# Performance work log

Hardware: AMD Instinct MI355X
Metric: run time of the kernel (lower is better)

## Reference

```python
import jax, jax.numpy as jnp
import numpy as np

# CrossAttention (DFFNet): 1x1 convs produce q,k from depth and v from rgb;
# full dense attention over hw spatial tokens: softmax(q^T k) then v @ mask^T.

def setup_inputs() -> dict:
    key = jax.random.key(0)
    ks = jax.random.split(key, 8)
    B, C, H, W = 4, 256, 64, 64
    Cqk = C // 8  # ratio=8 -> 32
    s = 0.02
    return {
        "rgb":   jax.random.normal(ks[0], (B, C, H, W), jnp.float32),
        "depth": jax.random.normal(ks[1], (B, C, H, W), jnp.float32),
        "Wq": jax.random.normal(ks[2], (Cqk, C), jnp.float32) * s,
        "bq": jax.random.normal(ks[3], (Cqk,), jnp.float32) * s,
        "Wk": jax.random.normal(ks[4], (Cqk, C), jnp.float32) * s,
        "bk": jax.random.normal(ks[5], (Cqk,), jnp.float32) * s,
        "Wv": jax.random.normal(ks[6], (C, C), jnp.float32) * s,
        "bv": jax.random.normal(ks[7], (C,), jnp.float32) * s,
    }


def reference(rgb, depth, Wq, bq, Wk, bk, Wv, bv):
    B, C, H, W = rgb.shape
    hw = H * W
    d = depth.reshape(B, C, hw)   # [B, C, hw]
    r = rgb.reshape(B, C, hw)     # [B, C, hw]
    # 1x1 convs == channel-mixing linear maps
    q = jnp.einsum('oc,bcn->bon', Wq, d) + bq[None, :, None]  # [B, Cqk, hw]
    k = jnp.einsum('oc,bcn->bon', Wk, d) + bk[None, :, None]  # [B, Cqk, hw]
    v = jnp.einsum('oc,bcn->bon', Wv, r) + bv[None, :, None]  # [B, C, hw]
    # scores: q^T k -> [B, hw, hw], softmax over last dim
    scores = jnp.einsum('bcn,bcm->bnm', q, k)
    mask = jax.nn.softmax(scores, axis=-1)
    # feat = v @ mask^T  -> [B, C, hw]
    feat = jnp.einsum('bcm,bnm->bcn', v, mask)
    return feat.reshape(B, C, H, W)
```

## Files before the change

### kernel.cpp

```cpp
#include <hip/hip_runtime.h>
#include <stdint.h>

#define L2E 1.44269504088896340736f

typedef _Float16 half8 __attribute__((ext_vector_type(8)));
typedef float floatx4 __attribute__((ext_vector_type(4)));

static __device__ __forceinline__ unsigned short f32_to_f16u(float f) {
  union { _Float16 h; unsigned short s; } cv; cv.h = (_Float16)f; return cv.s;
}

static __device__ __forceinline__ float fast_exp2(float x) {
  float r;
  asm("v_exp_f32 %0, %1" : "=v"(r) : "v"(x));
  return r;
}

typedef __attribute__((address_space(3))) unsigned int as3_uint;
typedef __attribute__((address_space(1))) const unsigned int as1_cuint;

static __device__ __forceinline__ void async16(const void* g, void* l) {
  __builtin_amdgcn_global_load_lds((as1_cuint*)g, (as3_uint*)l, 16, 0, 0);
}

__global__ __launch_bounds__(256) void proj_kernel(
    const float* __restrict__ rgb,
    const float* __restrict__ depth,
    const float* __restrict__ Wq, const float* __restrict__ bq,
    const float* __restrict__ Wk, const float* __restrict__ bk,
    const float* __restrict__ Wv, const float* __restrict__ bv,
    unsigned short* __restrict__ qT,
    unsigned short* __restrict__ kT,
    unsigned short* __restrict__ v)
{
  __shared__ __align__(16) unsigned short sX[256 * 76];
  __shared__ __align__(16) unsigned short sW[32 * 256];

  const int n0 = blockIdx.x * 64;
  const int b  = blockIdx.y;
  const int z  = blockIdx.z;
  const int t  = threadIdx.x;
  const int w  = t >> 6;
  const int lane = t & 63;
  const int l15 = lane & 15;
  const int q4  = lane >> 4;

  const float* X = (z == 0) ? depth : rgb;
  const float* xb = X + (size_t)b * 256 * 4096 + n0;

#pragma unroll
  for (int i = 0; i < 8; i++) {
    int h = i * 256 + t;
    int c = h >> 3, oct = h & 7;
    const float* src = xb + (size_t)c * 4096 + oct * 8;
    float4 x0 = *(const float4*)src;
    float4 x1 = *(const float4*)(src + 4);
    half8 hh;
    hh[0] = (_Float16)x0.x; hh[1] = (_Float16)x0.y; hh[2] = (_Float16)x0.z; hh[3] = (_Float16)x0.w;
    hh[4] = (_Float16)x1.x; hh[5] = (_Float16)x1.y; hh[6] = (_Float16)x1.z; hh[7] = (_Float16)x1.w;
    *(half8*)&sX[c * 76 + oct * 8] = hh;
  }
  __syncthreads();

  half8 a8[8];
#pragma unroll
  for (int ks = 0; ks < 8; ks++) {
#pragma unroll
    for (int j = 0; j < 8; j++) {
      a8[ks][j] = *(const _Float16*)&sX[(ks * 32 + q4 * 8 + j) * 76 + 16 * w + l15];
    }
  }

  const int ns = (z == 0) ? 2 : 4;
  for (int s = 0; s < ns; s++) {
    const int colbase = (z == 0) ? 0 : (z - 1) * 128 + s * 32;
    __syncthreads();

#pragma unroll
    for (int i = 0; i < 4; i++) {
      int L = i * 256 + t;
      int og = L >> 5;
      int phys = L & 31;
      int ci = phys ^ (og & 7);
      const float* wr;
      if (z == 0) wr = ((s == 0) ? Wq : Wk) + (size_t)og * 256;
      else        wr = Wv + (size_t)(colbase + og) * 256;
      float4 w0 = *(const float4*)(wr + ci * 8);
      float4 w1 = *(const float4*)(wr + ci * 8 + 4);
      half8 h;
      h[0] = (_Float16)w0.x; h[1] = (_Float16)w0.y; h[2] = (_Float16)w0.z; h[3] = (_Float16)w0.w;
      h[4] = (_Float16)w1.x; h[5] = (_Float16)w1.y; h[6] = (_Float16)w1.z; h[7] = (_Float16)w1.w;
      *(half8*)&sW[(size_t)L * 8] = h;
    }

    float bias2[2];
#pragma unroll
    for (int ct = 0; ct < 2; ct++) {
      int og = ct * 16 + l15;
      if (z == 0) bias2[ct] = (s == 0) ? bq[og] : bk[og];
      else        bias2[ct] = bv[colbase + og];
    }
    __syncthreads();

    floatx4 acc2[2];
    acc2[0] = (floatx4){0.f, 0.f, 0.f, 0.f};
    acc2[1] = (floatx4){0.f, 0.f, 0.f, 0.f};

#pragma unroll
    for (int ks = 0; ks < 8; ks++) {
      const int ci = ks * 4 + q4;
#pragma unroll
      for (int ct = 0; ct < 2; ct++) {
        int og = ct * 16 + l15;
        half8 bf = *(const half8*)&sW[og * 256 + ((ci ^ (og & 7)) * 8)];
        acc2[ct] = __builtin_amdgcn_mfma_f32_16x16x32_f16(a8[ks], bf, acc2[ct], 0, 0, 0);
      }
    }

    __syncthreads();

    if (z == 0) {
#pragma unroll
      for (int ct = 0; ct < 2; ct++) {
        int og = ct * 16 + l15;
#pragma unroll
        for (int r = 0; r < 4; r++) {
          int n = n0 + 16 * w + q4 * 4 + r;
          unsigned short hv = f32_to_f16u(acc2[ct][r] + bias2[ct]);
          if (s == 0) qT[((size_t)b * 4096 + n) * 32 + og] = hv;
          else        kT[((size_t)b * 4096 + n) * 32 + og] = hv;
        }
      }
    } else {
      unsigned short* tile = sW;
#pragma unroll
      for (int ct = 0; ct < 2; ct++) {
#pragma unroll
        for (int r = 0; r < 4; r++) {
          int co_l = ct * 16 + l15;
          int nl = 16 * w + q4 * 4 + r;
          tile[co_l * 72 + nl] = f32_to_f16u(acc2[ct][r] + bias2[ct]);
        }
      }
      __syncthreads();
      {
        int co_l = t >> 3;
        int ch = t & 7;
        int4 val = *(const int4*)&tile[co_l * 72 + ch * 8];
        *(int4*)&v[((size_t)b * 256 + colbase + co_l) * 4096 + n0 + ch * 8] = val;
      }
    }
  }
}

static __device__ __forceinline__ void stage_v(
    const unsigned short* __restrict__ vB, unsigned char* sbase,
    int m0, int t, int w)
{
#pragma unroll
  for (int j = 0; j < 4; j++) {
    int lin = j * 256 + t;
    int c = lin >> 2;
    int p = lin & 3;
    int lc = p ^ ((c >> 1) & 3);
    async16(&vB[(size_t)c * 4096 + m0 + lc * 8], sbase + j * 4096 + w * 1024);
  }
}

__global__ __launch_bounds__(256, 4) void attn_kernel(
    const unsigned short* __restrict__ qT,
    const unsigned short* __restrict__ kT,
    const unsigned short* __restrict__ v,
    unsigned short* __restrict__ Op,
    float* __restrict__ lW)
{
  __shared__ __align__(16) unsigned char smem[37888];
  unsigned short* sP = (unsigned short*)(smem + 32768);

  const int o = blockIdx.x;
  const int n0 = ((o >> 3) & 63) * 64;
  const int p  = (o & 7) | ((o >> 9) << 3);
  const int b  = p & 3;
  const int chunk = p >> 2;
  const int t  = threadIdx.x;
  const int w  = t >> 6;
  const int lane = t & 63;
  const int l15 = lane & 15;
  const int q4  = lane >> 4;

  half8 aq = *(const half8*)(qT + ((size_t)b * 4096 + n0 + 16 * w + l15) * 32 + q4 * 8);

  const unsigned short* vB = v + (size_t)b * 256 * 4096;
  const unsigned short* kL = kT + (size_t)b * 4096 * 32 + (size_t)l15 * 32 + q4 * 8;
  unsigned short* sPw = sP + w * 640;

  float lsum[4] = {0.f, 0.f, 0.f, 0.f};
  floatx4 acc[16];
#pragma unroll
  for (int ct = 0; ct < 16; ct++) acc[ct] = (floatx4){0.f, 0.f, 0.f, 0.f};
  const floatx4 zf = (floatx4){0.f, 0.f, 0.f, 0.f};

  const int mbase = chunk * 1024;

  stage_v(vB, smem, mbase, t, w);
  half8 kc0 = *(const half8*)(kL + (size_t)mbase * 32);
  half8 kc1 = *(const half8*)(kL + (size_t)(mbase + 16) * 32);

  int bufoff = 0;
  for (int it = 0; it < 32; ++it) {
    const int m0 = mbase + it * 32;
    half8 kn0 = kc0, kn1 = kc1;
    if (it < 31) {
      stage_v(vB, smem + (bufoff ^ 16384), m0 + 32, t, w);
      kn0 = *(const half8*)(kL + (size_t)(m0 + 32) * 32);
      kn1 = *(const half8*)(kL + (size_t)(m0 + 48) * 32);
      asm volatile("s_waitcnt vmcnt(6)" ::: "memory");
    } else {
      asm volatile("s_waitcnt vmcnt(0)" ::: "memory");
    }

    floatx4 s0 = __builtin_amdgcn_mfma_f32_16x16x32_f16(aq, kc0, zf, 0, 0, 0);
    floatx4 s1 = __builtin_amdgcn_mfma_f32_16x16x32_f16(aq, kc1, zf, 0, 0, 0);

    float p0[4], p1[4];
#pragma unroll
    for (int r = 0; r < 4; r++) {
      p0[r] = fast_exp2(s0[r] * L2E);
      p1[r] = fast_exp2(s1[r] * L2E);
      lsum[r] += p0[r] + p1[r];
    }
#pragma unroll
    for (int r = 0; r < 4; r++) {
      int row = q4 * 4 + r;
      sPw[row * 40 + l15]      = f32_to_f16u(p0[r]);
      sPw[row * 40 + 16 + l15] = f32_to_f16u(p1[r]);
    }
    asm volatile("s_waitcnt lgkmcnt(0)" ::: "memory");

    __builtin_amdgcn_s_barrier();
    asm volatile("s_waitcnt lgkmcnt(0)" ::: "memory");

    half8 ap[4];
#pragma unroll
    for (int nt = 0; nt < 4; nt++)
      ap[nt] = *(const half8*)&sP[nt * 640 + l15 * 40 + q4 * 8];

    const unsigned short* sVb = (const unsigned short*)(smem + bufoff);
#pragma unroll
    for (int ct = 0; ct < 4; ct++) {
      int co = w * 64 + ct * 16 + l15;
      half8 bv8 = *(const half8*)&sVb[co * 32 + ((q4 ^ ((co >> 1) & 3)) * 8)];
#pragma unroll
      for (int nt = 0; nt < 4; nt++)
        acc[ct * 4 + nt] = __builtin_amdgcn_mfma_f32_16x16x32_f16(ap[nt], bv8, acc[ct * 4 + nt], 0, 0, 0);
    }
    asm volatile("s_waitcnt lgkmcnt(0)" ::: "memory");
    __builtin_amdgcn_s_barrier();

    kc0 = kn0; kc1 = kn1;
    bufoff ^= 16384;
  }

#pragma unroll
  for (int off = 1; off < 16; off <<= 1) {
#pragma unroll
    for (int r = 0; r < 4; r++) lsum[r] += __shfl_xor(lsum[r], off);
  }
  if (l15 == 0) {
#pragma unroll
    for (int r = 0; r < 4; r++)
      lW[((size_t)chunk * 4 + b) * 4096 + n0 + 16 * w + q4 * 4 + r] = lsum[r];
  }

  unsigned short* sO = (unsigned short*)smem;
#pragma unroll
  for (int pass = 0; pass < 2; pass++) {
    __syncthreads();
    if ((w >> 1) == pass) {
#pragma unroll
      for (int ct = 0; ct < 4; ct++) {
        int co_l = (w & 1) * 64 + ct * 16 + l15;
#pragma unroll
        for (int nt = 0; nt < 4; nt++) {
#pragma unroll
          for (int r = 0; r < 4; r++) {
            int nl = nt * 16 + q4 * 4 + r;
            sO[co_l * 72 + nl] = f32_to_f16u(acc[ct * 4 + nt][r]);
          }
        }
      }
    }
    __syncthreads();
#pragma unroll
    for (int s = 0; s < 4; s++) {
      int co_l = s * 32 + (t >> 3);
      int ch = t & 7;
      int4 val = *(const int4*)&sO[co_l * 72 + ch * 8];
      *(int4*)&Op[(((size_t)chunk * 4 + b) * 256 + pass * 128 + co_l) * 4096 + n0 + ch * 8] = val;
    }
  }
}

__global__ __launch_bounds__(256) void combine_kernel(
    const unsigned short* __restrict__ Op,
    const float* __restrict__ lW,
    float* __restrict__ out)
{
  const int t = threadIdx.x;
  const int b = blockIdx.y;
  const size_t n8 = (size_t)blockIdx.x * 2048 + (size_t)t * 8;
  const int co0 = blockIdx.z * 4;

  float sum[8] = {0.f, 0.f, 0.f, 0.f, 0.f, 0.f, 0.f, 0.f};
#pragma unroll
  for (int ch = 0; ch < 4; ch++) {
    const float* lp = lW + ((size_t)ch * 4 + b) * 4096 + n8;
    float4 a0 = *(const float4*)lp;
    float4 a1 = *(const float4*)(lp + 4);
    sum[0] += a0.x; sum[1] += a0.y; sum[2] += a0.z; sum[3] += a0.w;
    sum[4] += a1.x; sum[5] += a1.y; sum[6] += a1.z; sum[7] += a1.w;
  }
  float rl[8];
#pragma unroll
  for (int i = 0; i < 8; i++) rl[i] = 1.0f / sum[i];

#pragma unroll
  for (int cc = 0; cc < 4; cc++) {
    int co = co0 + cc;
    float o[8] = {0.f, 0.f, 0.f, 0.f, 0.f, 0.f, 0.f, 0.f};
#pragma unroll
    for (int ch = 0; ch < 4; ch++) {
      half8 hv = *(const half8*)&Op[(((size_t)ch * 4 + b) * 256 + co) * 4096 + n8];
#pragma unroll
      for (int i = 0; i < 8; i++) o[i] += (float)hv[i];
    }
    float* op = out + ((size_t)b * 256 + co) * 4096 + n8;
    float4 r0, r1;
    r0.x = o[0] * rl[0]; r0.y = o[1] * rl[1]; r0.z = o[2] * rl[2]; r0.w = o[3] * rl[3];
    r1.x = o[4] * rl[4]; r1.y = o[5] * rl[5]; r1.z = o[6] * rl[6]; r1.w = o[7] * rl[7];
    *(float4*)op = r0;
    *(float4*)(op + 4) = r1;
  }
}

extern "C" void kernel_launch(void* const* d_in, const int* in_sizes, int n_in,
                              void* d_out, int out_size, void* d_ws, size_t ws_size,
                              hipStream_t stream) {
  const float* rgb   = (const float*)d_in[0];
  const float* depth = (const float*)d_in[1];
  const float* Wq    = (const float*)d_in[2];
  const float* bq    = (const float*)d_in[3];
  const float* Wk    = (const float*)d_in[4];
  const float* bk    = (const float*)d_in[5];
  const float* Wv    = (const float*)d_in[6];
  const float* bv    = (const float*)d_in[7];
  float* out = (float*)d_out;

  unsigned short* qT = (unsigned short*)d_ws;
  unsigned short* kT = qT + (size_t)4 * 4096 * 32;
  unsigned short* vW = kT + (size_t)4 * 4096 * 32;
  unsigned short* Op = vW + (size_t)4 * 256 * 4096;
  float* lW = (float*)(Op + (size_t)4 * 4 * 256 * 4096);

  dim3 pg(64, 4, 3);
  proj_kernel<<<pg, 256, 0, stream>>>(rgb, depth, Wq, bq, Wk, bk, Wv, bv, qT, kT, vW);
  attn_kernel<<<dim3(1024, 1, 1), 256, 0, stream>>>(qT, kT, vW, Op, lW);
  dim3 cg(2, 4, 64);
  combine_kernel<<<cg, 256, 0, stream>>>(Op, lW, out);
}
```

Measured before the change: 160.3 us.

## Keep softmax probabilities in registers by transposing QK MFMA, drop P shared-memory roundtrip

Computes the score tile as K·Q so each lane's exp outputs already sit in the operand layout of a 16x16x16 MFMA. The probabilities then feed the PV product straight from registers instead of going through a shared-memory P buffer. Each wave now covers all 256 output channels for its own 16 query rows, with one barrier per iteration instead of two. The tradeoffs are twice as many smaller MFMAs, more V reads from shared memory per wave, and a full vmcnt(0) wait at the top of each iteration, which weakens the prefetch overlap.

```diff
diff --git a/kernel.cpp b/kernel.cpp
--- a/kernel.cpp
+++ b/kernel.cpp
@@ -4,6 +4,7 @@
 #define L2E 1.44269504088896340736f
 
 typedef _Float16 half8 __attribute__((ext_vector_type(8)));
+typedef _Float16 half4 __attribute__((ext_vector_type(4)));
 typedef float floatx4 __attribute__((ext_vector_type(4)));
 
 static __device__ __forceinline__ unsigned short f32_to_f16u(float f) {
@@ -174,8 +175,7 @@
     unsigned short* __restrict__ Op,
     float* __restrict__ lW)
 {
-  __shared__ __align__(16) unsigned char smem[37888];
-  unsigned short* sP = (unsigned short*)(smem + 32768);
+  __shared__ __align__(16) unsigned char smem[36864];
 
   const int o = blockIdx.x;
   const int n0 = ((o >> 3) & 63) * 64;
@@ -192,9 +192,8 @@
 
   const unsigned short* vB = v + (size_t)b * 256 * 4096;
   const unsigned short* kL = kT + (size_t)b * 4096 * 32 + (size_t)l15 * 32 + q4 * 8;
-  unsigned short* sPw = sP + w * 640;
-
-  float lsum[4] = {0.f, 0.f, 0.f, 0.f};
+
+  float lsum = 0.f;
   floatx4 acc[16];
 #pragma unroll
   for (int ct = 0; ct < 16; ct++) acc[ct] = (floatx4){0.f, 0.f, 0.f, 0.f};
@@ -206,98 +205,67 @@
   half8 kc0 = *(const half8*)(kL + (size_t)mbase * 32);
   half8 kc1 = *(const half8*)(kL + (size_t)(mbase + 16) * 32);
 
-  int bufoff = 0;
+  const int sw = (l15 >> 1) & 3;
+  const int offA = (((q4 >> 1) ^ sw) << 3) + ((q4 & 1) << 2);
+  const int offB = ((((q4 >> 1) + 2) ^ sw) << 3) + ((q4 & 1) << 2);
+
   for (int it = 0; it < 32; ++it) {
     const int m0 = mbase + it * 32;
-    half8 kn0 = kc0, kn1 = kc1;
+    asm volatile("s_waitcnt vmcnt(0)" ::: "memory");
+    __builtin_amdgcn_s_barrier();
+    asm volatile("" ::: "memory");
+
+    if (it < 31) stage_v(vB, smem + ((~it & 1) << 14), m0 + 32, t, w);
+
+    floatx4 s0 = __builtin_amdgcn_mfma_f32_16x16x32_f16(kc0, aq, zf, 0, 0, 0);
+    floatx4 s1 = __builtin_amdgcn_mfma_f32_16x16x32_f16(kc1, aq, zf, 0, 0, 0);
     if (it < 31) {
-      stage_v(vB, smem + (bufoff ^ 16384), m0 + 32, t, w);
-      kn0 = *(const half8*)(kL + (size_t)(m0 + 32) * 32);
-      kn1 = *(const half8*)(kL + (size_t)(m0 + 48) * 32);
-      asm volatile("s_waitcnt vmcnt(6)" ::: "memory");
-    } else {
-      asm volatile("s_waitcnt vmcnt(0)" ::: "memory");
-    }
-
-    floatx4 s0 = __builtin_amdgcn_mfma_f32_16x16x32_f16(aq, kc0, zf, 0, 0, 0);
-    floatx4 s1 = __builtin_amdgcn_mfma_f32_16x16x32_f16(aq, kc1, zf, 0, 0, 0);
-
-    float p0[4], p1[4];
+      kc0 = *(const half8*)(kL + (size_t)(m0 + 32) * 32);
+      kc1 = *(const half8*)(kL + (size_t)(m0 + 48) * 32);
+    }
+
+    half4 pa, pb;
 #pragma unroll
     for (int r = 0; r < 4; r++) {
-      p0[r] = fast_exp2(s0[r] * L2E);
-      p1[r] = fast_exp2(s1[r] * L2E);
-      lsum[r] += p0[r] + p1[r];
-    }
+      float p0 = fast_exp2(s0[r] * L2E);
+      float p1 = fast_exp2(s1[r] * L2E);
+      lsum += p0 + p1;
+      pa[r] = (_Float16)p0;
+      pb[r] = (_Float16)p1;
+    }
+
+    const unsigned short* sVb = (const unsigned short*)(smem + ((it & 1) << 14));
+#pragma unroll
+    for (int ct = 0; ct < 16; ct++) {
+      int co = ct * 16 + l15;
+      half4 va = *(const half4*)&sVb[co * 32 + offA];
+      half4 vb = *(const half4*)&sVb[co * 32 + offB];
+      acc[ct] = __builtin_amdgcn_mfma_f32_16x16x16f16(va, pa, acc[ct], 0, 0, 0);
+      acc[ct] = __builtin_amdgcn_mfma_f32_16x16x16f16(vb, pb, acc[ct], 0, 0, 0);
+    }
+  }
+
+  lsum += __shfl_xor(lsum, 16);
+  lsum += __shfl_xor(lsum, 32);
+  if (q4 == 0)
+    lW[((size_t)chunk * 4 + b) * 4096 + n0 + 16 * w + l15] = lsum;
+
+  unsigned short* sO = (unsigned short*)smem;
+  __syncthreads();
+#pragma unroll
+  for (int ct = 0; ct < 16; ct++) {
 #pragma unroll
     for (int r = 0; r < 4; r++) {
-      int row = q4 * 4 + r;
-      sPw[row * 40 + l15]      = f32_to_f16u(p0[r]);
-      sPw[row * 40 + 16 + l15] = f32_to_f16u(p1[r]);
-    }
-    asm volatile("s_waitcnt lgkmcnt(0)" ::: "memory");
-
-    __builtin_amdgcn_s_barrier();
-    asm volatile("s_waitcnt lgkmcnt(0)" ::: "memory");
-
-    half8 ap[4];
-#pragma unroll
-    for (int nt = 0; nt < 4; nt++)
-      ap[nt] = *(const half8*)&sP[nt * 640 + l15 * 40 + q4 * 8];
-
-    const unsigned short* sVb = (const unsigned short*)(smem + bufoff);
-#pragma unroll
-    for (int ct = 0; ct < 4; ct++) {
-      int co = w * 64 + ct * 16 + l15;
-      half8 bv8 = *(const half8*)&sVb[co * 32 + ((q4 ^ ((co >> 1) & 3)) * 8)];
-#pragma unroll
-      for (int nt = 0; nt < 4; nt++)
-        acc[ct * 4 + nt] = __builtin_amdgcn_mfma_f32_16x16x32_f16(ap[nt], bv8, acc[ct * 4 + nt], 0, 0, 0);
-    }
-    asm volatile("s_waitcnt lgkmcnt(0)" ::: "memory");
-    __builtin_amdgcn_s_barrier();
-
-    kc0 = kn0; kc1 = kn1;
-    bufoff ^= 16384;
-  }
-
-#pragma unroll
-  for (int off = 1; off < 16; off <<= 1) {
-#pragma unroll
-    for (int r = 0; r < 4; r++) lsum[r] += __shfl_xor(lsum[r], off);
-  }
-  if (l15 == 0) {
-#pragma unroll
-    for (int r = 0; r < 4; r++)
-      lW[((size_t)chunk * 4 + b) * 4096 + n0 + 16 * w + q4 * 4 + r] = lsum[r];
-  }
-
-  unsigned short* sO = (unsigned short*)smem;
-#pragma unroll
-  for (int pass = 0; pass < 2; pass++) {
-    __syncthreads();
-    if ((w >> 1) == pass) {
-#pragma unroll
-      for (int ct = 0; ct < 4; ct++) {
-        int co_l = (w & 1) * 64 + ct * 16 + l15;
-#pragma unroll
-        for (int nt = 0; nt < 4; nt++) {
-#pragma unroll
-          for (int r = 0; r < 4; r++) {
-            int nl = nt * 16 + q4 * 4 + r;
-            sO[co_l * 72 + nl] = f32_to_f16u(acc[ct * 4 + nt][r]);
-          }
-        }
-      }
-    }
-    __syncthreads();
-#pragma unroll
-    for (int s = 0; s < 4; s++) {
-      int co_l = s * 32 + (t >> 3);
-      int ch = t & 7;
-      int4 val = *(const int4*)&sO[co_l * 72 + ch * 8];
-      *(int4*)&Op[(((size_t)chunk * 4 + b) * 256 + pass * 128 + co_l) * 4096 + n0 + ch * 8] = val;
-    }
+      sO[(ct * 16 + q4 * 4 + r) * 72 + 16 * w + l15] = f32_to_f16u(acc[ct][r]);
+    }
+  }
+  __syncthreads();
+#pragma unroll
+  for (int i = 0; i < 8; i++) {
+    int co_l = i * 32 + (t >> 3);
+    int ch = t & 7;
+    int4 val = *(const int4*)&sO[co_l * 72 + ch * 8];
+    *(int4*)&Op[(((size_t)chunk * 4 + b) * 256 + co_l) * 4096 + n0 + ch * 8] = val;
   }
 }
 
```

New measurement: 174.2 us. 1.09x slower.
